# Performance work log

Hardware: AMD Instinct MI355X
Metric: run time of the kernel (lower is better)

The kernel has to match this reference:

```python
import jax, jax.numpy as jnp
import numpy as np

E = 65536      # num edges
T = 262144     # num triplets
H = 128        # hidden_channels
D = 64         # int_emb_size
C = 8          # basis_emb_size
NR = 6         # num_radial
NS = 7         # num_spherical
NB = 6         # len(bt_list) = num_BT + 1
BT_LIST = (-1, 0, 1, 2, 3, 4)
NBS = 1        # num_before_skip (also used for after-skip list in original code)


def setup_inputs() -> dict:
    key = jax.random.key(0)
    ks = iter(jax.random.split(key, 40))
    s = 0.05
    p = lambda shape: jax.random.normal(next(ks), shape, dtype=jnp.float32) * s
    inp = dict(
        x=jax.random.normal(next(ks), (E, H), dtype=jnp.float32),
        rbf=jax.random.normal(next(ks), (E, NR), dtype=jnp.float32),
        sbf=jax.random.normal(next(ks), (T, NS * NR), dtype=jnp.float32),
        idx_kj=jax.random.randint(next(ks), (T,), 0, E),
        idx_ji=jax.random.randint(next(ks), (T,), 0, E),
        bt=jax.random.randint(next(ks), (E,), 0, 5),
        lambda_d=1,
        alpha=jnp.float32(0.7),
        # per-branch stacked weights (6 branches)
        W_kj=p((NB, H, H)), b_kj=jnp.zeros((NB, H), jnp.float32),
        W_rbf1=p((NB, NR, C)), W_rbf2=p((NB, C, H)),
        W_sbf1=p((NB, NS * NR, C)), W_sbf2=p((NB, C, D)),
        W_down=p((NB, H, D)),
        W_ji=p((H, H)), b_ji=jnp.zeros((H,), jnp.float32),
        W_up=p((D, H)),
        rb1_w=p((NBS, H, H)), rb1_b=jnp.zeros((NBS, H), jnp.float32),
        rb2_w=p((NBS, H, H)), rb2_b=jnp.zeros((NBS, H), jnp.float32),
        W_lin=p((H, H)), b_lin=jnp.zeros((H,), jnp.float32),
        ra1_w=p((NBS, H, H)), ra1_b=jnp.zeros((NBS, H), jnp.float32),
        ra2_w=p((NBS, H, H)), ra2_b=jnp.zeros((NBS, H), jnp.float32),
    )
    return inp


def reference(x, rbf, sbf, idx_kj, idx_ji, bt, lambda_d, alpha,
              W_kj, b_kj, W_rbf1, W_rbf2, W_sbf1, W_sbf2, W_down,
              W_ji, b_ji, W_up, rb1_w, rb1_b, rb2_w, rb2_b,
              W_lin, b_lin, ra1_w, ra1_b, ra2_w, ra2_b):
    act = jax.nn.silu

    x_ji = act(x @ W_ji + b_ji)                                  # [E,H]

    # per-branch edge transforms, vectorized over the 6 branches (axis b)
    tmp = act(jnp.einsum('eh,bhg->beg', x, W_kj) + b_kj[:, None, :])   # [B,E,H]
    rbf_p = jnp.einsum('er,brc->bec', rbf, W_rbf1)                     # [B,E,C]
    rbf_p = jnp.einsum('bec,bcg->beg', rbf_p, W_rbf2)                  # [B,E,H]
    tmp = tmp * rbf_p
    down = act(jnp.einsum('beh,bhd->bed', tmp, W_down))                # [B,E,D]

    sbf_p = jnp.einsum('ts,bsc->btc', sbf, W_sbf1)                     # [B,T,C]
    sbf_p = jnp.einsum('btc,bcd->btd', sbf_p, W_sbf2)                  # [B,T,D]

    spe = down[:, idx_kj, :] * sbf_p                                   # [B,T,D]

    # last branch scattered with weight alpha
    x_kj_tot = alpha * jax.ops.segment_sum(spe[-1], idx_ji, num_segments=E)

    # per band-type masked scatter with weight (1 - alpha)
    bt_trip = bt[idx_kj]                                               # [T]
    for b, btv in enumerate(BT_LIST):
        m = (bt_trip == btv).astype(x.dtype)[:, None]
        x_kj_tot = x_kj_tot + (1.0 - alpha) * jax.ops.segment_sum(
            spe[b] * m, idx_ji, num_segments=E)

    x_kj = act(x_kj_tot @ W_up)                                        # [E,H]
    h = x_ji + x_kj
    for i in range(rb1_w.shape[0]):
        h = h + act(act(h @ rb1_w[i] + rb1_b[i]) @ rb2_w[i] + rb2_b[i])
    h = act(h @ W_lin + b_lin) + x
    for i in range(ra1_w.shape[0]):
        h = h + act(act(h @ ra1_w[i] + ra1_b[i]) @ ra2_w[i] + ra2_b[i])
    return h
```

## Files before the change

kernel.cpp:

```cpp
#include <hip/hip_runtime.h>
#include <hip/hip_bf16.h>
#include <stdint.h>

typedef __bf16 bf16_t;
typedef bf16_t bf16x8 __attribute__((ext_vector_type(8)));
typedef bf16_t bf16x2 __attribute__((ext_vector_type(2)));
typedef float f32x4 __attribute__((ext_vector_type(4)));

#define E_N 65536
#define T_N 262144

__device__ __forceinline__ float silu_f(float v) {
  return v / (1.0f + __expf(-v));
}

__device__ __forceinline__ int permrow(int n) {
  return (n & ~31) | ((n & 1) << 4) | ((n & 30) >> 1);
}

__device__ __forceinline__ uint32_t pack_bf16(float a, float b) {
  union { bf16x2 h; uint32_t u; } u;
  u.h[0] = (bf16_t)a; u.h[1] = (bf16_t)b;
  return u.u;
}

__device__ __forceinline__ float2 ubf2f(uint32_t v) {
  union { uint32_t u; bf16x2 h; } c; c.u = v;
  return make_float2((float)c.h[0], (float)c.h[1]);
}

__device__ __forceinline__ void atomic_pk_add_bf16(bf16_t* addr, uint32_t val) {
  asm volatile("global_atomic_pk_add_bf16 %0, %1, off" :: "v"(addr), "v"(val) : "memory");
}

template<int KI, int NTJ, int BS>
__device__ __forceinline__ void gemm_bg(const bf16_t* A, const bf16_t* __restrict__ Bg,
                                        int mb, int nb, int l16, int q,
                                        f32x4 (&acc)[2][NTJ]) {
  bf16x8 bfr[KI][NTJ];
  const bf16_t* bp = Bg + (nb + l16) * BS + q * 8;
#pragma unroll
  for (int kt = 0; kt < KI; ++kt)
#pragma unroll
    for (int tj = 0; tj < NTJ; ++tj)
      bfr[kt][tj] = *(const bf16x8*)(bp + tj * 16 * BS + kt * 32);
#pragma unroll
  for (int kt = 0; kt < KI; ++kt) {
    const int sw = ((kt * 4 + q) ^ l16) << 3;
    bf16x8 a0 = *(const bf16x8*)(A + ((mb + l16) << 7) + sw);
    bf16x8 a1 = *(const bf16x8*)(A + ((mb + 16 + l16) << 7) + sw);
#pragma unroll
    for (int tj = 0; tj < NTJ; ++tj) {
      acc[0][tj] = __builtin_amdgcn_mfma_f32_16x16x32_bf16(a0, bfr[kt][tj], acc[0][tj], 0, 0, 0);
      acc[1][tj] = __builtin_amdgcn_mfma_f32_16x16x32_bf16(a1, bfr[kt][tj], acc[1][tj], 0, 0, 0);
    }
  }
}

template<int C4>
__device__ __forceinline__ void stage_x(bf16_t* dst, const float* src, int tid) {
  const float4* g = (const float4*)src;
#pragma unroll
  for (int i = tid; i < 64 * C4; i += 256) {
    const int row = i / C4, c4 = i % C4;
    float4 v = g[i];
    bf16_t t[4] = {(bf16_t)v.x, (bf16_t)v.y, (bf16_t)v.z, (bf16_t)v.w};
    *(uint2*)(dst + (row << 7) + ((((c4 >> 1) ^ (row & 15)) << 3) | ((c4 & 1) << 2))) =
        *(const uint2*)t;
  }
}

__device__ __forceinline__ void stage_xkj(bf16_t* dst, const bf16_t* src, int tid) {
  const uint4* g = (const uint4*)src;
#pragma unroll
  for (int i = tid; i < 64 * 8; i += 256) {
    const int row = i >> 3, k8 = i & 7;
    *(uint4*)(dst + (row << 7) + ((k8 ^ (row & 15)) << 3)) = g[i];
  }
}

__global__ void prep_kernel(
    const float* __restrict__ W_ji, const float* __restrict__ W_kj,
    const float* __restrict__ W_down, const float* __restrict__ W_up,
    const float* __restrict__ rb1, const float* __restrict__ rb2,
    const float* __restrict__ W_lin, const float* __restrict__ ra1,
    const float* __restrict__ ra2, const float* __restrict__ W_rbf1,
    const float* __restrict__ W_rbf2, const float* __restrict__ W_sbf1,
    const float* __restrict__ W_sbf2,
    bf16_t* __restrict__ wjiT, bf16_t* __restrict__ wkjT,
    bf16_t* __restrict__ wdownT, bf16_t* __restrict__ wupT,
    bf16_t* __restrict__ rb1T, bf16_t* __restrict__ rb2T,
    bf16_t* __restrict__ linT, bf16_t* __restrict__ ra1T,
    bf16_t* __restrict__ ra2T, bf16_t* __restrict__ wcb,
    bf16_t* __restrict__ wsT)
{
  const int tid = threadIdx.x;
  const int bx = blockIdx.x;
  if (bx < 112) {
    const int c = bx * 256 + tid;
    const float* src; bf16_t* dst; int n, k8, N, K;
    if (c < 22528) {
      const int m = c >> 11, w = c & 2047;
      n = w >> 4; k8 = w & 15; N = 128; K = 128;
      if (m == 0)      { src = W_ji;  dst = wjiT; }
      else if (m <= 5) { src = W_kj + m * 16384; dst = wkjT + (m - 1) * 16384; }
      else if (m == 6) { src = rb1;   dst = rb1T; }
      else if (m == 7) { src = rb2;   dst = rb2T; }
      else if (m == 8) { src = W_lin; dst = linT; }
      else if (m == 9) { src = ra1;   dst = ra1T; }
      else             { src = ra2;   dst = ra2T; }
    } else if (c < 27648) {
      const int m = (c - 22528) >> 10, w = (c - 22528) & 1023;
      n = w >> 4; k8 = w & 15; N = 64; K = 128;
      src = W_down + (m + 1) * 8192; dst = wdownT + m * 8192;
    } else {
      const int w = c - 27648;
      n = w >> 3; k8 = w & 7; N = 128; K = 64;
      src = W_up; dst = wupT;
    }
    bf16_t t[8];
#pragma unroll
    for (int j = 0; j < 8; ++j) t[j] = (bf16_t)src[(k8 * 8 + j) * N + n];
    *(uint4*)(dst + permrow(n) * K + k8 * 8) = *(const uint4*)t;
  } else if (bx < 115) {
    const int o = (bx - 112) * 256 + tid;
    if (o < 640) {
      const int slot = o >> 7, n = o & 127;
      const int b = slot + 1;
      bf16_t t[32];
#pragma unroll
      for (int k = 0; k < 32; ++k) t[k] = (bf16_t)0.f;
#pragma unroll
      for (int r = 0; r < 6; ++r) {
        float s = 0.f;
#pragma unroll
        for (int c = 0; c < 8; ++c)
          s += W_rbf1[b * 48 + r * 8 + c] * W_rbf2[b * 1024 + c * 128 + n];
        t[r] = (bf16_t)s;
      }
      bf16_t* dst = wcb + slot * 4096 + permrow(n) * 32;
#pragma unroll
      for (int g = 0; g < 4; ++g) *(uint4*)(dst + g * 8) = *(const uint4*)(t + g * 8);
    }
  } else {
    const int o = (bx - 115) * 256 + tid;
    if (o < 320) {
      const int slot = o >> 6, j = o & 63;
      const int b = slot + 1;
      bf16_t t[64];
#pragma unroll
      for (int s = 0; s < 64; ++s) {
        float v = 0.f;
        if (s < 42) {
#pragma unroll
          for (int c = 0; c < 8; ++c)
            v += W_sbf1[b * 336 + s * 8 + c] * W_sbf2[b * 512 + c * 64 + j];
        }
        t[s] = (bf16_t)v;
      }
      bf16_t* dst = wsT + (slot * 64 + permrow(j)) * 64;
#pragma unroll
      for (int g = 0; g < 8; ++g) *(uint4*)(dst + g * 8) = *(const uint4*)(t + g * 8);
    }
  }
}

__global__ __launch_bounds__(256, 3)
void edge_kernel(const float* __restrict__ x, const float* __restrict__ rbf,
                 const float* __restrict__ b_kj, const float* __restrict__ b_ji,
                 const bf16_t* __restrict__ wjiT, const bf16_t* __restrict__ wkjT,
                 const bf16_t* __restrict__ wdownT, const bf16_t* __restrict__ wcb,
                 bf16_t* __restrict__ x_ji_out, bf16_t* __restrict__ down)
{
  __shared__ bf16_t xA[64 * 128];
  __shared__ bf16_t tmpA[64 * 128];
  __shared__ bf16_t rbfA[64 * 32];
  __shared__ float biasS[128];

  const int tid = threadIdx.x;
  const int lane = tid & 63, wv = tid >> 6;
  const int q = lane >> 4, l16 = lane & 15;
  const int mb = (wv >> 1) * 32, nb = (wv & 1) * 64;
  const int R = blockIdx.x * 64;
  const int br = blockIdx.y;

  stage_x<32>(xA, x + (size_t)R * 128, tid);
  if (tid < 128) biasS[tid] = (br == 0) ? b_ji[tid] : b_kj[br * 128 + tid];
  if (br != 0 && tid < 64) {
    const float* rg = rbf + (size_t)(R + tid) * 6;
    bf16_t t[8] = {(bf16_t)rg[0], (bf16_t)rg[1], (bf16_t)rg[2],
                   (bf16_t)rg[3], (bf16_t)rg[4], (bf16_t)rg[5],
                   (bf16_t)0.f, (bf16_t)0.f};
    const uint4 z = {0, 0, 0, 0};
    bf16_t* dst = rbfA + tid * 32;
#pragma unroll
    for (int g = 0; g < 4; ++g) *(uint4*)(dst + g * 8) = z;
    *(uint4*)(dst + ((tid & 3) << 3)) = *(const uint4*)t;
  }
  __syncthreads();

  const bf16_t* WB = (br == 0) ? wjiT : wkjT + (size_t)(br - 1) * 16384;
  f32x4 acc[2][4] = {};
  gemm_bg<4, 4, 128>(xA, WB, mb, nb, l16, q, acc);

  if (br == 0) {
#pragma unroll
    for (int ti = 0; ti < 2; ++ti)
#pragma unroll
      for (int r = 0; r < 4; ++r) {
        const int row = mb + ti * 16 + q * 4 + r;
#pragma unroll
        for (int gl = 0; gl < 2; ++gl) {
          const int col0 = nb + gl * 32 + 2 * l16;
          const float2 b2 = *(const float2*)&biasS[col0];
          *(uint32_t*)&x_ji_out[(size_t)(R + row) * 128 + col0] =
              pack_bf16(silu_f(acc[ti][2 * gl][r] + b2.x),
                        silu_f(acc[ti][2 * gl + 1][r] + b2.y));
        }
      }
    return;
  }

  f32x4 accr[2][4] = {};
  {
    const int sw = (q ^ (l16 & 3)) << 3;
    bf16x8 a0 = *(const bf16x8*)(rbfA + ((mb + l16) << 5) + sw);
    bf16x8 a1 = *(const bf16x8*)(rbfA + ((mb + 16 + l16) << 5) + sw);
    const bf16_t* wb = wcb + (size_t)(br - 1) * 4096 + (nb + l16) * 32 + q * 8;
    bf16x8 bf0 = *(const bf16x8*)(wb);
    bf16x8 bf1 = *(const bf16x8*)(wb + 16 * 32);
    bf16x8 bf2 = *(const bf16x8*)(wb + 32 * 32);
    bf16x8 bf3 = *(const bf16x8*)(wb + 48 * 32);
    accr[0][0] = __builtin_amdgcn_mfma_f32_16x16x32_bf16(a0, bf0, accr[0][0], 0, 0, 0);
    accr[1][0] = __builtin_amdgcn_mfma_f32_16x16x32_bf16(a1, bf0, accr[1][0], 0, 0, 0);
    accr[0][1] = __builtin_amdgcn_mfma_f32_16x16x32_bf16(a0, bf1, accr[0][1], 0, 0, 0);
    accr[1][1] = __builtin_amdgcn_mfma_f32_16x16x32_bf16(a1, bf1, accr[1][1], 0, 0, 0);
    accr[0][2] = __builtin_amdgcn_mfma_f32_16x16x32_bf16(a0, bf2, accr[0][2], 0, 0, 0);
    accr[1][2] = __builtin_amdgcn_mfma_f32_16x16x32_bf16(a1, bf2, accr[1][2], 0, 0, 0);
    accr[0][3] = __builtin_amdgcn_mfma_f32_16x16x32_bf16(a0, bf3, accr[0][3], 0, 0, 0);
    accr[1][3] = __builtin_amdgcn_mfma_f32_16x16x32_bf16(a1, bf3, accr[1][3], 0, 0, 0);
  }

#pragma unroll
  for (int ti = 0; ti < 2; ++ti)
#pragma unroll
    for (int r = 0; r < 4; ++r) {
      const int row = mb + ti * 16 + q * 4 + r;
#pragma unroll
      for (int gl = 0; gl < 2; ++gl) {
        const int col0 = nb + gl * 32 + 2 * l16;
        const float2 b2 = *(const float2*)&biasS[col0];
        const float v0 = silu_f(acc[ti][2 * gl][r] + b2.x) * accr[ti][2 * gl][r];
        const float v1 = silu_f(acc[ti][2 * gl + 1][r] + b2.y) * accr[ti][2 * gl + 1][r];
        *(uint32_t*)&tmpA[(row << 7) + ((((col0 >> 3) ^ (row & 15)) << 3) | (col0 & 7))] =
            pack_bf16(v0, v1);
      }
    }
  __syncthreads();

  const int nb2 = (wv & 1) * 32;
  f32x4 acc2[2][2] = {};
  gemm_bg<4, 2, 128>(tmpA, wdownT + (size_t)(br - 1) * 8192, mb, nb2, l16, q, acc2);
#pragma unroll
  for (int ti = 0; ti < 2; ++ti)
#pragma unroll
    for (int r = 0; r < 4; ++r) {
      const int row = mb + ti * 16 + q * 4 + r;
      const int col0 = nb2 + 2 * l16;
      *(uint32_t*)&down[((size_t)(R + row) * 5 + (br - 1)) * 64 + col0] =
          pack_bf16(silu_f(acc2[ti][0][r]), silu_f(acc2[ti][1][r]));
    }
}

__global__ __launch_bounds__(256, 3)
void triplet_kernel(const float* __restrict__ sbf, const int* __restrict__ idx_kj,
                    const int* __restrict__ idx_ji, const int* __restrict__ bt,
                    const float* __restrict__ alpha_p, const bf16_t* __restrict__ wsT,
                    const bf16_t* __restrict__ down, bf16_t* __restrict__ xkj)
{
  __shared__ bf16_t s_sbf[64 * 64];
  __shared__ bf16_t spC[64 * 344];
  __shared__ int s_kj[64], s_ji[64], s_bs[64];

  const int tid = threadIdx.x;
  const int lane = tid & 63, wv = tid >> 6;
  const int q = lane >> 4, l16 = lane & 15;
  const int base = blockIdx.x * 64;

  if (tid < 64) {
    const int kj = idx_kj[base + tid];
    s_kj[tid] = kj;
    s_ji[tid] = idx_ji[base + tid];
    s_bs[tid] = bt[kj];
  }
#pragma unroll
  for (int it = 0; it < 2; ++it) {
    const int i = tid + it * 256;
    const int row = i >> 3, k8 = i & 7;
    const float* sg = sbf + (size_t)(base + row) * 42 + k8 * 8;
    bf16_t t[8];
#pragma unroll
    for (int jj = 0; jj < 8; ++jj)
      t[jj] = (k8 * 8 + jj < 42) ? (bf16_t)sg[jj] : (bf16_t)0.f;
    *(uint4*)(s_sbf + (row << 6) + ((k8 ^ (row & 7)) << 3)) = *(const uint4*)t;
  }
  __syncthreads();

  const int mb = (wv & 1) * 32;
  const int tb0 = (wv >> 1) * 10;
  f32x4 acc[2][10] = {};
#pragma unroll
  for (int kt = 0; kt < 2; ++kt) {
    const int sw = (((kt << 2) + q) ^ (l16 & 7)) << 3;
    bf16x8 a0 = *(const bf16x8*)(s_sbf + ((mb + l16) << 6) + sw);
    bf16x8 a1 = *(const bf16x8*)(s_sbf + ((mb + 16 + l16) << 6) + sw);
    const bf16_t* bp = wsT + (tb0 * 16 + l16) * 64 + (kt << 5) + (q << 3);
#pragma unroll
    for (int tj = 0; tj < 10; ++tj) {
      bf16x8 b = *(const bf16x8*)(bp + tj * 1024);
      acc[0][tj] = __builtin_amdgcn_mfma_f32_16x16x32_bf16(a0, b, acc[0][tj], 0, 0, 0);
      acc[1][tj] = __builtin_amdgcn_mfma_f32_16x16x32_bf16(a1, b, acc[1][tj], 0, 0, 0);
    }
  }
#pragma unroll
  for (int ti = 0; ti < 2; ++ti)
#pragma unroll
    for (int r = 0; r < 4; ++r) {
      const int row = mb + ti * 16 + q * 4 + r;
#pragma unroll
      for (int tp = 0; tp < 5; ++tp) {
        const int t0 = tb0 + 2 * tp;
        const int col = (t0 >> 2) * 64 + (((t0 & 3) >> 1) << 5) + 2 * l16;
        *(uint32_t*)&spC[row * 344 + col] =
            pack_bf16(acc[ti][2 * tp][r], acc[ti][2 * tp + 1][r]);
      }
    }
  __syncthreads();

  const float alpha = alpha_p[0];
  const float oma = 1.f - alpha;
  const int hf = lane >> 5;
  const int j0 = (lane & 31) * 2;

  uint32_t G5[8], GB[8];
#pragma unroll
  for (int ii = 0; ii < 8; ++ii) {
    const int t = wv * 16 + ii * 2 + hf;
    const bf16_t* dr = down + (size_t)s_kj[t] * 320;
    G5[ii] = *(const uint32_t*)(dr + 256 + j0);
    GB[ii] = *(const uint32_t*)(dr + s_bs[t] * 64 + j0);
  }
#pragma unroll
  for (int ii = 0; ii < 8; ++ii) {
    const int t = wv * 16 + ii * 2 + hf;
    const int slot = s_bs[t];
    const int ji = s_ji[t];
    const float2 d5 = ubf2f(*(const uint32_t*)&spC[t * 344 + 256 + j0]);
    const float2 db = ubf2f(*(const uint32_t*)&spC[t * 344 + slot * 64 + j0]);
    const float2 g5 = ubf2f(G5[ii]);
    const float2 gb = ubf2f(GB[ii]);
    const float r0 = alpha * g5.x * d5.x + oma * gb.x * db.x;
    const float r1 = alpha * g5.y * d5.y + oma * gb.y * db.y;
    atomic_pk_add_bf16(&xkj[(size_t)ji * 64 + j0], pack_bf16(r0, r1));
  }
}

__global__ __launch_bounds__(256, 3)
void epi_kernel(const float* __restrict__ x, const bf16_t* __restrict__ x_ji,
                const bf16_t* __restrict__ xkj,
                const bf16_t* __restrict__ wupT,
                const bf16_t* __restrict__ rb1T, const float* __restrict__ rb1_b,
                const bf16_t* __restrict__ rb2T, const float* __restrict__ rb2_b,
                const bf16_t* __restrict__ linT, const float* __restrict__ lin_b,
                const bf16_t* __restrict__ ra1T, const float* __restrict__ ra1_b,
                const bf16_t* __restrict__ ra2T, const float* __restrict__ ra2_b,
                float* __restrict__ out)
{
  __shared__ bf16_t bufA[64 * 128];
  __shared__ bf16_t bufB[64 * 128];
  __shared__ float biasAll[5 * 128];

  const int tid = threadIdx.x;
  const int lane = tid & 63, wv = tid >> 6;
  const int q = lane >> 4, l16 = lane & 15;
  const int mb = (wv >> 1) * 32, nb = (wv & 1) * 64;
  const int R = blockIdx.x * 64;

  stage_xkj(bufA, xkj + (size_t)R * 64, tid);
  if (tid < 128) {
    biasAll[tid]       = rb1_b[tid];
    biasAll[128 + tid] = rb2_b[tid];
    biasAll[256 + tid] = lin_b[tid];
    biasAll[384 + tid] = ra1_b[tid];
    biasAll[512 + tid] = ra2_b[tid];
  }
  __syncthreads();

  f32x4 hreg[2][4];
  {
    f32x4 acc[2][4] = {};
    gemm_bg<2, 4, 64>(bufA, wupT, mb, nb, l16, q, acc);
#pragma unroll
    for (int ti = 0; ti < 2; ++ti)
#pragma unroll
      for (int r = 0; r < 4; ++r) {
        const int row = mb + ti * 16 + q * 4 + r;
#pragma unroll
        for (int gl = 0; gl < 2; ++gl) {
          const int col0 = nb + gl * 32 + 2 * l16;
          union { uint32_t u; bf16x2 h; } xj;
          xj.u = *(const uint32_t*)&x_ji[(size_t)(R + row) * 128 + col0];
          const float h0 = (float)xj.h[0] + silu_f(acc[ti][2 * gl][r]);
          const float h1 = (float)xj.h[1] + silu_f(acc[ti][2 * gl + 1][r]);
          hreg[ti][2 * gl][r] = h0;
          hreg[ti][2 * gl + 1][r] = h1;
          *(uint32_t*)&bufB[(row << 7) + ((((col0 >> 3) ^ (row & 15)) << 3) | (col0 & 7))] =
              pack_bf16(h0, h1);
        }
      }
  }

#define EPI_STAGE(ASRC, WPTR, BROW, BODY)                                        \
  __syncthreads();                                                               \
  {                                                                              \
    f32x4 acc[2][4] = {};                                                        \
    gemm_bg<4, 4, 128>(ASRC, WPTR, mb, nb, l16, q, acc);                         \
    _Pragma("unroll")                                                            \
    for (int ti = 0; ti < 2; ++ti)                                               \
      _Pragma("unroll")                                                          \
      for (int r = 0; r < 4; ++r) {                                              \
        const int row = mb + ti * 16 + q * 4 + r;                                \
        _Pragma("unroll")                                                        \
        for (int gl = 0; gl < 2; ++gl) {                                         \
          const int col0 = nb + gl * 32 + 2 * l16;                               \
          const float2 b2 = *(const float2*)&biasAll[BROW * 128 + col0];         \
          const float g0 = acc[ti][2 * gl][r] + b2.x;                            \
          const float g1 = acc[ti][2 * gl + 1][r] + b2.y;                        \
          BODY                                                                   \
        }                                                                        \
      }                                                                          \
  }

  EPI_STAGE(bufB, rb1T, 0, {
    *(uint32_t*)&bufA[(row << 7) + ((((col0 >> 3) ^ (row & 15)) << 3) | (col0 & 7))] =
        pack_bf16(silu_f(g0), silu_f(g1));
  })

  EPI_STAGE(bufA, rb2T, 1, {
    const float h0 = hreg[ti][2 * gl][r] + silu_f(g0);
    const float h1 = hreg[ti][2 * gl + 1][r] + silu_f(g1);
    hreg[ti][2 * gl][r] = h0; hreg[ti][2 * gl + 1][r] = h1;
    *(uint32_t*)&bufB[(row << 7) + ((((col0 >> 3) ^ (row & 15)) << 3) | (col0 & 7))] =
        pack_bf16(h0, h1);
  })

  EPI_STAGE(bufB, linT, 2, {
    const float2 xv = *(const float2*)&x[(size_t)(R + row) * 128 + col0];
    const float h0 = silu_f(g0) + xv.x;
    const float h1 = silu_f(g1) + xv.y;
    hreg[ti][2 * gl][r] = h0; hreg[ti][2 * gl + 1][r] = h1;
    *(uint32_t*)&bufA[(row << 7) + ((((col0 >> 3) ^ (row & 15)) << 3) | (col0 & 7))] =
        pack_bf16(h0, h1);
  })

  EPI_STAGE(bufA, ra1T, 3, {
    *(uint32_t*)&bufB[(row << 7) + ((((col0 >> 3) ^ (row & 15)) << 3) | (col0 & 7))] =
        pack_bf16(silu_f(g0), silu_f(g1));
  })

  EPI_STAGE(bufB, ra2T, 4, {
    float2 o;
    o.x = hreg[ti][2 * gl][r] + silu_f(g0);
    o.y = hreg[ti][2 * gl + 1][r] + silu_f(g1);
    *(float2*)&out[(size_t)(R + row) * 128 + col0] = o;
  })
#undef EPI_STAGE
}

extern "C" void kernel_launch(void* const* d_in, const int* in_sizes, int n_in,
                              void* d_out, int out_size, void* d_ws, size_t ws_size,
                              hipStream_t stream)
{
  (void)in_sizes; (void)n_in; (void)out_size; (void)ws_size;
  const float* x      = (const float*)d_in[0];
  const float* rbf    = (const float*)d_in[1];
  const float* sbf    = (const float*)d_in[2];
  const int*   idx_kj = (const int*)d_in[3];
  const int*   idx_ji = (const int*)d_in[4];
  const int*   bt     = (const int*)d_in[5];
  const float* alpha  = (const float*)d_in[7];
  const float* W_kj   = (const float*)d_in[8];
  const float* b_kj   = (const float*)d_in[9];
  const float* W_rbf1 = (const float*)d_in[10];
  const float* W_rbf2 = (const float*)d_in[11];
  const float* W_sbf1 = (const float*)d_in[12];
  const float* W_sbf2 = (const float*)d_in[13];
  const float* W_down = (const float*)d_in[14];
  const float* W_ji   = (const float*)d_in[15];
  const float* b_ji   = (const float*)d_in[16];
  const float* W_up   = (const float*)d_in[17];
  const float* rb1_w  = (const float*)d_in[18];
  const float* rb1_b  = (const float*)d_in[19];
  const float* rb2_w  = (const float*)d_in[20];
  const float* rb2_b  = (const float*)d_in[21];
  const float* W_lin  = (const float*)d_in[22];
  const float* b_lin  = (const float*)d_in[23];
  const float* ra1_w  = (const float*)d_in[24];
  const float* ra1_b  = (const float*)d_in[25];
  const float* ra2_w  = (const float*)d_in[26];
  const float* ra2_b  = (const float*)d_in[27];

  char* ws = (char*)d_ws;
  bf16_t* down   = (bf16_t*)(ws);
  bf16_t* x_ji   = (bf16_t*)(ws + 41943040);
  bf16_t* xkj    = (bf16_t*)(ws + 58720256);
  char* wbase    = ws + 75497472;
  bf16_t* wjiT   = (bf16_t*)(wbase + 0);
  bf16_t* wkjT   = (bf16_t*)(wbase + 32768);
  bf16_t* wdownT = (bf16_t*)(wbase + 196608);
  bf16_t* wupT   = (bf16_t*)(wbase + 278528);
  bf16_t* rb1T   = (bf16_t*)(wbase + 294912);
  bf16_t* rb2T   = (bf16_t*)(wbase + 327680);
  bf16_t* linT   = (bf16_t*)(wbase + 360448);
  bf16_t* ra1T   = (bf16_t*)(wbase + 393216);
  bf16_t* ra2T   = (bf16_t*)(wbase + 425984);
  bf16_t* wcb    = (bf16_t*)(wbase + 458752);
  bf16_t* wsT    = (bf16_t*)(wbase + 499712);

  hipMemsetAsync(xkj, 0, (size_t)E_N * 64 * 2, stream);
  prep_kernel<<<117, 256, 0, stream>>>(W_ji, W_kj, W_down, W_up, rb1_w, rb2_w,
                                       W_lin, ra1_w, ra2_w, W_rbf1, W_rbf2,
                                       W_sbf1, W_sbf2,
                                       wjiT, wkjT, wdownT, wupT, rb1T, rb2T,
                                       linT, ra1T, ra2T, wcb, wsT);
  edge_kernel<<<dim3(E_N / 64, 6), 256, 0, stream>>>(x, rbf, b_kj, b_ji, wjiT,
                                                     wkjT, wdownT, wcb, x_ji, down);
  triplet_kernel<<<T_N / 64, 256, 0, stream>>>(sbf, idx_kj, idx_ji, bt, alpha,
                                               wsT, down, xkj);
  epi_kernel<<<E_N / 64, 256, 0, stream>>>(x, x_ji, xkj, wupT, rb1T, rb1_b,
                                           rb2T, rb2_b, linT, b_lin,
                                           ra1T, ra1_b, ra2T, ra2_b,
                                           (float*)d_out);
}
```

Baseline: 392.5 us.

## Pre-convert x to bf16 once and stage edge GEMM weights in LDS

A new kernel converts x from fp32 to bf16 once, so the six branch blocks of the edge kernel each read half the bytes and skip per-block conversion. The edge kernel now copies the full W_kj/W_ji matrix and later W_down into swizzled shared memory and reads B fragments from LDS, instead of loading them from global memory into registers. The rbf-combined weight fragments are prefetched before staging. LDS use grows, so launch bounds drop from 3 to 2 blocks per SM, trading occupancy for less global weight traffic. It also adds one extra kernel launch and a 16 MB workspace buffer.

```diff
diff --git a/kernel.cpp b/kernel.cpp
--- a/kernel.cpp
+++ b/kernel.cpp
@@ -31,6 +31,31 @@
 
 __device__ __forceinline__ void atomic_pk_add_bf16(bf16_t* addr, uint32_t val) {
   asm volatile("global_atomic_pk_add_bf16 %0, %1, off" :: "v"(addr), "v"(val) : "memory");
+}
+
+__device__ __forceinline__ bf16x8 pack8(float4 a, float4 b) {
+  union { bf16x8 v; uint32_t u[4]; } z;
+  z.u[0] = pack_bf16(a.x, a.y); z.u[1] = pack_bf16(a.z, a.w);
+  z.u[2] = pack_bf16(b.x, b.y); z.u[3] = pack_bf16(b.z, b.w);
+  return z.v;
+}
+
+template<int KI, int NTJ>
+__device__ __forceinline__ void gemm_ls(const bf16_t* A, const bf16_t* B,
+                                        int mb, int nb, int l16, int q,
+                                        f32x4 (&acc)[2][NTJ]) {
+#pragma unroll
+  for (int kt = 0; kt < KI; ++kt) {
+    const int sw = ((kt * 4 + q) ^ l16) << 3;
+    bf16x8 a0 = *(const bf16x8*)(A + ((mb + l16) << 7) + sw);
+    bf16x8 a1 = *(const bf16x8*)(A + ((mb + 16 + l16) << 7) + sw);
+#pragma unroll
+    for (int tj = 0; tj < NTJ; ++tj) {
+      bf16x8 b = *(const bf16x8*)(B + ((nb + tj * 16 + l16) << 7) + sw);
+      acc[0][tj] = __builtin_amdgcn_mfma_f32_16x16x32_bf16(a0, b, acc[0][tj], 0, 0, 0);
+      acc[1][tj] = __builtin_amdgcn_mfma_f32_16x16x32_bf16(a1, b, acc[1][tj], 0, 0, 0);
+    }
+  }
 }
 
 template<int KI, int NTJ, int BS>
@@ -57,16 +82,14 @@
   }
 }
 
-template<int C4>
-__device__ __forceinline__ void stage_x(bf16_t* dst, const float* src, int tid) {
-  const float4* g = (const float4*)src;
-#pragma unroll
-  for (int i = tid; i < 64 * C4; i += 256) {
-    const int row = i / C4, c4 = i % C4;
-    float4 v = g[i];
-    bf16_t t[4] = {(bf16_t)v.x, (bf16_t)v.y, (bf16_t)v.z, (bf16_t)v.w};
-    *(uint2*)(dst + (row << 7) + ((((c4 >> 1) ^ (row & 15)) << 3) | ((c4 & 1) << 2))) =
-        *(const uint2*)t;
+template<int ROWS>
+__device__ __forceinline__ void stage_sw(bf16_t* dst, const bf16_t* __restrict__ src,
+                                         int tid) {
+  const uint4* g = (const uint4*)src;
+#pragma unroll
+  for (int i = tid; i < ROWS * 16; i += 256) {
+    const int row = i >> 4, k8 = i & 15;
+    *(uint4*)(dst + (row << 7) + ((k8 ^ (row & 15)) << 3)) = g[i];
   }
 }
 
@@ -165,14 +188,22 @@
   }
 }
 
-__global__ __launch_bounds__(256, 3)
-void edge_kernel(const float* __restrict__ x, const float* __restrict__ rbf,
+__global__ void xbf_kernel(const float* __restrict__ x, bf16_t* __restrict__ xbf) {
+  const int i = blockIdx.x * 256 + threadIdx.x;
+  float4 a = ((const float4*)x)[2 * i];
+  float4 b = ((const float4*)x)[2 * i + 1];
+  ((bf16x8*)xbf)[i] = pack8(a, b);
+}
+
+__global__ __launch_bounds__(256, 2)
+void edge_kernel(const bf16_t* __restrict__ xbf, const float* __restrict__ rbf,
                  const float* __restrict__ b_kj, const float* __restrict__ b_ji,
                  const bf16_t* __restrict__ wjiT, const bf16_t* __restrict__ wkjT,
                  const bf16_t* __restrict__ wdownT, const bf16_t* __restrict__ wcb,
                  bf16_t* __restrict__ x_ji_out, bf16_t* __restrict__ down)
 {
   __shared__ bf16_t xA[64 * 128];
+  __shared__ bf16_t Wb[128 * 128];
   __shared__ bf16_t tmpA[64 * 128];
   __shared__ bf16_t rbfA[64 * 32];
   __shared__ float biasS[128];
@@ -184,7 +215,15 @@
   const int R = blockIdx.x * 64;
   const int br = blockIdx.y;
 
-  stage_x<32>(xA, x + (size_t)R * 128, tid);
+  bf16x8 wcf[4];
+  if (br != 0) {
+    const bf16_t* wb = wcb + (size_t)(br - 1) * 4096 + (nb + l16) * 32 + q * 8;
+#pragma unroll
+    for (int tj = 0; tj < 4; ++tj) wcf[tj] = *(const bf16x8*)(wb + tj * 16 * 32);
+  }
+
+  stage_sw<64>(xA, xbf + (size_t)R * 128, tid);
+  stage_sw<128>(Wb, (br == 0) ? wjiT : wkjT + (size_t)(br - 1) * 16384, tid);
   if (tid < 128) biasS[tid] = (br == 0) ? b_ji[tid] : b_kj[br * 128 + tid];
   if (br != 0 && tid < 64) {
     const float* rg = rbf + (size_t)(R + tid) * 6;
@@ -199,9 +238,8 @@
   }
   __syncthreads();
 
-  const bf16_t* WB = (br == 0) ? wjiT : wkjT + (size_t)(br - 1) * 16384;
   f32x4 acc[2][4] = {};
-  gemm_bg<4, 4, 128>(xA, WB, mb, nb, l16, q, acc);
+  gemm_ls<4, 4>(xA, Wb, mb, nb, l16, q, acc);
 
   if (br == 0) {
 #pragma unroll
@@ -223,22 +261,14 @@
 
   f32x4 accr[2][4] = {};
   {
-    const int sw = (q ^ (l16 & 3)) << 3;
-    bf16x8 a0 = *(const bf16x8*)(rbfA + ((mb + l16) << 5) + sw);
-    bf16x8 a1 = *(const bf16x8*)(rbfA + ((mb + 16 + l16) << 5) + sw);
-    const bf16_t* wb = wcb + (size_t)(br - 1) * 4096 + (nb + l16) * 32 + q * 8;
-    bf16x8 bf0 = *(const bf16x8*)(wb);
-    bf16x8 bf1 = *(const bf16x8*)(wb + 16 * 32);
-    bf16x8 bf2 = *(const bf16x8*)(wb + 32 * 32);
-    bf16x8 bf3 = *(const bf16x8*)(wb + 48 * 32);
-    accr[0][0] = __builtin_amdgcn_mfma_f32_16x16x32_bf16(a0, bf0, accr[0][0], 0, 0, 0);
-    accr[1][0] = __builtin_amdgcn_mfma_f32_16x16x32_bf16(a1, bf0, accr[1][0], 0, 0, 0);
-    accr[0][1] = __builtin_amdgcn_mfma_f32_16x16x32_bf16(a0, bf1, accr[0][1], 0, 0, 0);
-    accr[1][1] = __builtin_amdgcn_mfma_f32_16x16x32_bf16(a1, bf1, accr[1][1], 0, 0, 0);
-    accr[0][2] = __builtin_amdgcn_mfma_f32_16x16x32_bf16(a0, bf2, accr[0][2], 0, 0, 0);
-    accr[1][2] = __builtin_amdgcn_mfma_f32_16x16x32_bf16(a1, bf2, accr[1][2], 0, 0, 0);
-    accr[0][3] = __builtin_amdgcn_mfma_f32_16x16x32_bf16(a0, bf3, accr[0][3], 0, 0, 0);
-    accr[1][3] = __builtin_amdgcn_mfma_f32_16x16x32_bf16(a1, bf3, accr[1][3], 0, 0, 0);
+    const int swr = (q ^ (l16 & 3)) << 3;
+    bf16x8 a0 = *(const bf16x8*)(rbfA + ((mb + l16) << 5) + swr);
+    bf16x8 a1 = *(const bf16x8*)(rbfA + ((mb + 16 + l16) << 5) + swr);
+#pragma unroll
+    for (int tj = 0; tj < 4; ++tj) {
+      accr[0][tj] = __builtin_amdgcn_mfma_f32_16x16x32_bf16(a0, wcf[tj], accr[0][tj], 0, 0, 0);
+      accr[1][tj] = __builtin_amdgcn_mfma_f32_16x16x32_bf16(a1, wcf[tj], accr[1][tj], 0, 0, 0);
+    }
   }
 
 #pragma unroll
@@ -257,10 +287,12 @@
       }
     }
   __syncthreads();
+  stage_sw<64>(xA, wdownT + (size_t)(br - 1) * 8192, tid);
+  __syncthreads();
 
   const int nb2 = (wv & 1) * 32;
   f32x4 acc2[2][2] = {};
-  gemm_bg<4, 2, 128>(tmpA, wdownT + (size_t)(br - 1) * 8192, mb, nb2, l16, q, acc2);
+  gemm_ls<4, 2>(tmpA, xA, mb, nb2, l16, q, acc2);
 #pragma unroll
   for (int ti = 0; ti < 2; ++ti)
 #pragma unroll
@@ -514,7 +546,8 @@
   bf16_t* down   = (bf16_t*)(ws);
   bf16_t* x_ji   = (bf16_t*)(ws + 41943040);
   bf16_t* xkj    = (bf16_t*)(ws + 58720256);
-  char* wbase    = ws + 75497472;
+  bf16_t* xbf    = (bf16_t*)(ws + 67108864);
+  char* wbase    = ws + 83886080;
   bf16_t* wjiT   = (bf16_t*)(wbase + 0);
   bf16_t* wkjT   = (bf16_t*)(wbase + 32768);
   bf16_t* wdownT = (bf16_t*)(wbase + 196608);
@@ -533,7 +566,8 @@
                                        W_sbf1, W_sbf2,
                                        wjiT, wkjT, wdownT, wupT, rb1T, rb2T,
                                        linT, ra1T, ra2T, wcb, wsT);
-  edge_kernel<<<dim3(E_N / 64, 6), 256, 0, stream>>>(x, rbf, b_kj, b_ji, wjiT,
+  xbf_kernel<<<E_N * 128 / 8 / 256, 256, 0, stream>>>(x, xbf);
+  edge_kernel<<<dim3(E_N / 64, 6), 256, 0, stream>>>(xbf, rbf, b_kj, b_ji, wjiT,
                                                      wkjT, wdownT, wcb, x_ji, down);
   triplet_kernel<<<T_N / 64, 256, 0, stream>>>(sbf, idx_kj, idx_ji, bt, alpha,
                                                wsT, down, xkj);
```

After: 387.8 us. About the same (-1.2%).
